# Kernel tuning notes

Measured on AMD Instinct MI355X. Metric: run time of the kernel, lower is better.

The kernel has to match this reference:

```python
import jax, jax.numpy as jnp
import numpy as np

B, T, DIM, H, HD = 1, 4096, 1024, 8, 128
ATTN_SCALE = 0.12


def _rms_norm(x):
    # F.rms_norm with default eps = finfo(dtype).eps, no learned weight
    eps = jnp.asarray(jnp.finfo(x.dtype).eps, x.dtype)
    return x * jax.lax.rsqrt(jnp.mean(x * x, axis=-1, keepdims=True) + eps)


def _rotary(x):
    # x: [B, T, H, D]; half-rotary: last D/2 freqs are zero (identity)
    t, d = x.shape[1], x.shape[-1]
    freqs = (1.0 / 1024.0) ** jnp.linspace(0.0, 1.0, d // 4, dtype=jnp.float32)
    freqs = jnp.concatenate([freqs, jnp.zeros(d // 4, dtype=jnp.float32)])
    theta = jnp.arange(t, dtype=jnp.float32)[:, None] * freqs[None, :]  # [T, D/2]
    cos = jnp.cos(theta)[None, :, None, :]
    sin = jnp.sin(theta)[None, :, None, :]
    x1, x2 = jnp.split(x.astype(jnp.float32), 2, axis=-1)
    y = jnp.concatenate([x1 * cos + x2 * sin, -x1 * sin + x2 * cos], axis=-1)
    return y.astype(x.dtype)


def setup_inputs() -> dict:
    key = jax.random.key(0)
    k1, k2, k3, k4, k5 = jax.random.split(key, 5)
    std = 0.5 * DIM ** -0.5
    bound = (3.0 ** 0.5) * std
    x = jax.random.normal(k1, (B, T, DIM), dtype=jnp.float32)
    ve = jax.random.normal(k2, (B, T, DIM), dtype=jnp.float32)
    qkv_w = jax.random.uniform(k3, (3, H * HD, DIM), dtype=jnp.float32,
                               minval=-bound, maxval=bound)
    lambdas = jnp.array([0.5, 0.5], dtype=jnp.float32)
    # c_proj is zero-initialized in the source; use small random weights so the
    # output (and gradients) are non-trivial for correctness testing
    c_proj_w = jax.random.normal(k4, (DIM, H * HD), dtype=jnp.float32) * 0.02
    docs = jnp.sort(jax.random.randint(k5, (T,), 0, 8, dtype=jnp.int32))
    return {"x": x, "ve": ve, "qkv_w": qkv_w, "lambdas": lambdas,
            "c_proj_w": c_proj_w, "docs": docs}


def reference(x, ve, qkv_w, lambdas, c_proj_w, docs):
    b, t, _ = x.shape
    w = qkv_w.reshape(3 * H * HD, -1)              # [3*hdim, dim]
    qkv = (x @ w.T).reshape(b, t, 3, H, HD)        # chunk(3, dim=-2) == axis 2 here
    q, k, v = qkv[:, :, 0], qkv[:, :, 1], qkv[:, :, 2]
    q, k = _rms_norm(q), _rms_norm(k)
    q, k = _rotary(q), _rotary(k)
    v = lambdas[0] * v + lambdas[1] * ve.reshape(v.shape)
    # doc-causal mask: attend within the same document, causally
    i = jnp.arange(t)
    mask = (i[:, None] >= i[None, :]) & (docs[:, None] == docs[None, :])  # [T, T]
    scores = jnp.einsum('bihd,bjhd->bhij', q, k) * ATTN_SCALE
    scores = jnp.where(mask[None, None], scores, -jnp.inf)
    p = jax.nn.softmax(scores, axis=-1)
    y = jnp.einsum('bhij,bjhd->bihd', p, v).reshape(b, t, H * HD)
    return y @ c_proj_w.T
```

## Files before the change

### kernel.cpp

```cpp
#include <hip/hip_runtime.h>
#include <hip/hip_bf16.h>
#include <cstdint>

typedef __attribute__((ext_vector_type(8))) short sh8;
typedef __attribute__((ext_vector_type(4))) float f4;
typedef __attribute__((ext_vector_type(16))) float f16v;

#define T_SEQ 4096
#define DIMN  1024
#define NH    8
#define HDIM  128
#define NQKV  3072
#define ATTN_SCALE 0.12f

__device__ __forceinline__ ushort f2bf(float x) {
  __hip_bfloat16 b = __float2bfloat16(x);
  return *reinterpret_cast<ushort*>(&b);
}
__device__ __forceinline__ float bf2f(ushort u) {
  uint v = ((uint)u) << 16;
  float f;
  __builtin_memcpy(&f, &v, 4);
  return f;
}

#define GLDS16(g, l) \
  __builtin_amdgcn_global_load_lds((const __attribute__((address_space(1))) void*)(g), \
                                   (__attribute__((address_space(3))) void*)(l), 16, 0, 0)

template <int N>
__device__ __forceinline__ void wait_vmcnt() {
  if constexpr (N == 0)      asm volatile("s_waitcnt vmcnt(0)" ::: "memory");
  else if constexpr (N == 4) asm volatile("s_waitcnt vmcnt(4)" ::: "memory");
  else if constexpr (N == 8) asm volatile("s_waitcnt vmcnt(8)" ::: "memory");
  __builtin_amdgcn_sched_barrier(0);
}
#define BAR __builtin_amdgcn_s_barrier()

__global__ __launch_bounds__(256) void k_prep(const float* __restrict__ x,
                                              const float* __restrict__ qw,
                                              const float* __restrict__ cw,
                                              ushort* __restrict__ xb, ushort* __restrict__ wb,
                                              ushort* __restrict__ cbuf,
                                              const int* __restrict__ docs, int* __restrict__ dstart) {
  const int b = blockIdx.x;
  if (b < 8192) {
    const int i = b * 256 + threadIdx.x;
    const float* src;
    ushort* dst;
    int j;
    if (i < 1048576)       { src = x;  dst = xb;   j = i; }
    else if (i < 1835008)  { src = qw; dst = wb;   j = i - 1048576; }
    else                   { src = cw; dst = cbuf; j = i - 1835008; }
    float4 v = reinterpret_cast<const float4*>(src)[j];
    ushort4 o;
    o.x = f2bf(v.x); o.y = f2bf(v.y); o.z = f2bf(v.z); o.w = f2bf(v.w);
    reinterpret_cast<ushort4*>(dst)[j] = o;
  } else {
    const int i = (b - 8192) * 256 + threadIdx.x;
    if (i < T_SEQ) {
      int d = docs[i];
      int lo = 0, hi = i;
      while (lo < hi) { int mid = (lo + hi) >> 1; if (docs[mid] < d) lo = mid + 1; else hi = mid; }
      dstart[i] = lo;
    }
  }
}

__global__ __launch_bounds__(512, 2) void k_gemm256(const ushort* __restrict__ A,
                                                    const ushort* __restrict__ B,
                                                    ushort* __restrict__ C,
                                                    int N, int K) {
  __shared__ ushort lds[2][512 * 64];
  const int tid = threadIdx.x;
  const int lane = tid & 63;
  const int w = tid >> 6;
  const int l5 = lane >> 5;
  const int lr32 = lane & 31;
  const int wave_m = w >> 2, wave_n = w & 3;

  const int nb = (blockIdx.x & 7) * 24 + (blockIdx.x >> 3);
  const int m0 = (nb / 12) * 256;
  const int n0 = (nb % 12) * 256;

  f16v acc[4][2];
#pragma unroll
  for (int i = 0; i < 4; ++i)
#pragma unroll
    for (int j = 0; j < 2; ++j)
#pragma unroll
      for (int r = 0; r < 16; ++r) acc[i][j][r] = 0.f;

  const int NT = K >> 6;

  auto STAGE4 = [&](int buf, int t, int ug) {
    const int k0 = t << 6;
#pragma unroll
    for (int uu = 0; uu < 4; ++uu) {
      const int u = ug * 4 + uu;
      const int row = u * 64 + (tid >> 3);
      const int c = (tid & 7) ^ (row & 7);
      const ushort* src = (row < 256 ? A + (size_t)(m0 + row) * K
                                     : B + (size_t)(n0 + row - 256) * K) + k0 + c * 8;
      GLDS16(src, (char*)&lds[buf][0] + u * 8192 + w * 1024);
    }
  };

  STAGE4(0, 0, 0); STAGE4(0, 0, 1);
  wait_vmcnt<0>();
  BAR;

  int cur = 0;
  for (int t = 0; t < NT; ++t) {
    const bool more = (t + 1) < NT;
    const char* bb = (const char*)&lds[cur][0];

#define RD6(ks, a, b)                                                              \
    _Pragma("unroll") for (int mt = 0; mt < 4; ++mt) {                             \
      const int row = wave_m * 128 + mt * 32 + lr32;                               \
      a[mt] = *(const sh8*)(bb + row * 128 + ((((ks) * 2 + l5) ^ (row & 7)) * 16));\
    }                                                                              \
    _Pragma("unroll") for (int nt = 0; nt < 2; ++nt) {                             \
      const int row = 256 + wave_n * 64 + nt * 32 + lr32;                          \
      b[nt] = *(const sh8*)(bb + row * 128 + ((((ks) * 2 + l5) ^ (row & 7)) * 16));\
    }

#define MFMA8(a, b)                                                                \
    __builtin_amdgcn_s_setprio(1);                                                 \
    _Pragma("unroll") for (int mt = 0; mt < 4; ++mt)                               \
    _Pragma("unroll") for (int nt = 0; nt < 2; ++nt)                               \
      acc[mt][nt] = __builtin_amdgcn_mfma_f32_32x32x16_bf16(a[mt], b[nt],          \
                                                            acc[mt][nt], 0, 0, 0); \
    __builtin_amdgcn_s_setprio(0);

    {
      sh8 a[4], b[2];
      RD6(0, a, b)
      if (more) STAGE4(cur ^ 1, t + 1, 0);
      MFMA8(a, b)
    }
    {
      sh8 a[4], b[2];
      RD6(1, a, b)
      if (more) STAGE4(cur ^ 1, t + 1, 1);
      MFMA8(a, b)
    }
    BAR;
    {
      sh8 a[4], b[2];
      RD6(2, a, b)
      MFMA8(a, b)
    }
    {
      sh8 a[4], b[2];
      RD6(3, a, b)
      MFMA8(a, b)
    }
    if (more) wait_vmcnt<0>();
    BAR;
    cur ^= 1;
  }
#undef RD6
#undef MFMA8

#pragma unroll
  for (int mt = 0; mt < 4; ++mt)
#pragma unroll
    for (int nt = 0; nt < 2; ++nt) {
      const int gcol = n0 + wave_n * 64 + nt * 32 + lr32;
#pragma unroll
      for (int r = 0; r < 16; ++r) {
        const int grow = m0 + wave_m * 128 + mt * 32 + (r & 3) + 8 * (r >> 2) + 4 * l5;
        C[(size_t)grow * N + gcol] = f2bf(acc[mt][nt][r]);
      }
    }
}

__global__ __launch_bounds__(256) void k_gemm2(const ushort* __restrict__ A,
                                               const ushort* __restrict__ B,
                                               float* __restrict__ C,
                                               int N, int K, int gx) {
  constexpr int BM = 128, BN = 128;
  constexpr int CHA = BM * 4;
  constexpr int TILEB = (BM + BN) * 64;

  __shared__ __attribute__((aligned(16))) char lds[3 * TILEB];

  const int tid = threadIdx.x;
  const int lane = tid & 63;
  const int w = tid >> 6;
  const int l5 = lane >> 5;
  const int lr32 = lane & 31;
  const int wm = w >> 1, wn = w & 1;

  const int nwg = gridDim.x;
  const int nb = (blockIdx.x & 7) * (nwg >> 3) + (blockIdx.x >> 3);
  const int m0 = (nb / gx) * BM;
  const int n0 = (nb % gx) * BN;

  f16v acc[2][2];
#pragma unroll
  for (int i = 0; i < 2; ++i)
#pragma unroll
    for (int j = 0; j < 2; ++j)
#pragma unroll
      for (int r = 0; r < 16; ++r) acc[i][j][r] = 0.f;

  const int NT = K >> 5;

  auto STAGE = [&](int t, int buf) {
    const int k0 = t << 5;
#pragma unroll
    for (int l = 0; l < 4; ++l) {
      const int cb = (l * 4 + w) * 64;
      const int ch = cb + lane;
      const ushort* src;
      if (ch < CHA) {
        const int row = ch >> 2;
        const int cs = (ch & 3) ^ ((row >> 1) & 3);
        src = A + (size_t)(m0 + row) * K + k0 + cs * 8;
      } else {
        const int c2 = ch - CHA;
        const int row = c2 >> 2;
        const int cs = (c2 & 3) ^ ((row >> 1) & 3);
        src = B + (size_t)(n0 + row) * K + k0 + cs * 8;
      }
      GLDS16(src, lds + buf * TILEB + cb * 16);
    }
  };

  STAGE(0, 0);
  STAGE(1, 1);
  wait_vmcnt<4>();
  BAR;

  int bufc = 0;
  for (int t = 0; t < NT; ++t) {
    const bool more = (t + 2) < NT;
    if (more) STAGE(t + 2, bufc == 0 ? 2 : (bufc == 1 ? 0 : 1));

    const char* bb = lds + bufc * TILEB;
#pragma unroll
    for (int ks = 0; ks < 2; ++ks) {
      sh8 a[2], b[2];
#pragma unroll
      for (int mt = 0; mt < 2; ++mt) {
        const int row = wm * 64 + mt * 32 + lr32;
        a[mt] = *(const sh8*)(bb + row * 64 + (((ks * 2 + l5) ^ ((row >> 1) & 3)) * 16));
      }
#pragma unroll
      for (int nt = 0; nt < 2; ++nt) {
        const int row = wn * 64 + nt * 32 + lr32;
        b[nt] = *(const sh8*)(bb + BM * 64 + row * 64 + (((ks * 2 + l5) ^ ((row >> 1) & 3)) * 16));
      }
      __builtin_amdgcn_s_setprio(1);
#pragma unroll
      for (int mt = 0; mt < 2; ++mt)
#pragma unroll
        for (int nt = 0; nt < 2; ++nt)
          acc[mt][nt] = __builtin_amdgcn_mfma_f32_32x32x16_bf16(a[mt], b[nt], acc[mt][nt], 0, 0, 0);
      __builtin_amdgcn_s_setprio(0);
    }

    if (more) wait_vmcnt<4>();
    else      wait_vmcnt<0>();
    BAR;
    bufc = bufc == 2 ? 0 : bufc + 1;
  }

#pragma unroll
  for (int mt = 0; mt < 2; ++mt)
#pragma unroll
    for (int nt = 0; nt < 2; ++nt) {
      const int gcol = n0 + wn * 64 + nt * 32 + lr32;
#pragma unroll
      for (int r = 0; r < 16; ++r) {
        const int grow = m0 + wm * 64 + mt * 32 + (r & 3) + 8 * (r >> 2) + 4 * l5;
        __builtin_nontemporal_store(acc[mt][nt][r], &C[(size_t)grow * N + gcol]);
      }
    }
}

__global__ __launch_bounds__(256) void k_fuse(const ushort* __restrict__ qkvb,
                                              const float* __restrict__ ve,
                                              const float* __restrict__ lam,
                                              ushort* __restrict__ qh, ushort* __restrict__ kh,
                                              ushort* __restrict__ vh) {
  const int pair = blockIdx.x * 4 + (threadIdx.x >> 6);
  const int t = pair >> 3, h = pair & 7;
  const int l = threadIdx.x & 63;
  const ushort* base = qkvb + (size_t)t * NQKV + h * HDIM + 2 * l;
  uint qu = *reinterpret_cast<const uint*>(base);
  uint ku = *reinterpret_cast<const uint*>(base + 1024);
  uint vu = *reinterpret_cast<const uint*>(base + 2048);
  float q0 = bf2f((ushort)qu), q1 = bf2f((ushort)(qu >> 16));
  float k0 = bf2f((ushort)ku), k1 = bf2f((ushort)(ku >> 16));
  float v0 = bf2f((ushort)vu), v1 = bf2f((ushort)(vu >> 16));
  float sq = q0 * q0 + q1 * q1, sk = k0 * k0 + k1 * k1;
#pragma unroll
  for (int m = 1; m < 64; m <<= 1) { sq += __shfl_xor(sq, m); sk += __shfl_xor(sk, m); }
  const float eps = 1.1920928955078125e-07f;
  float rq = rsqrtf(sq * (1.f / 128.f) + eps);
  float rk = rsqrtf(sk * (1.f / 128.f) + eps);
  q0 *= rq; q1 *= rq; k0 *= rk; k1 *= rk;
  float c0 = 1.f, s0 = 0.f, c1 = 1.f, s1 = 0.f;
  if ((l & 31) < 16) {
    const int f0 = 2 * (l & 31);
    float fr0 = exp2f(-10.f * (float)f0 * (1.f / 31.f));
    float fr1 = exp2f(-10.f * (float)(f0 + 1) * (1.f / 31.f));
    sincosf((float)t * fr0, &s0, &c0);
    sincosf((float)t * fr1, &s1, &c1);
  }
  float qx0 = __shfl_xor(q0, 32), qx1 = __shfl_xor(q1, 32);
  float kx0 = __shfl_xor(k0, 32), kx1 = __shfl_xor(k1, 32);
  const float sgn = (l < 32) ? 1.f : -1.f;
  float qr0 = q0 * c0 + sgn * qx0 * s0;
  float qr1 = q1 * c1 + sgn * qx1 * s1;
  float kr0 = k0 * c0 + sgn * kx0 * s0;
  float kr1 = k1 * c1 + sgn * kx1 * s1;
  const float l0 = lam[0], l1 = lam[1];
  float2 vev = *reinterpret_cast<const float2*>(ve + (size_t)t * DIMN + h * HDIM + 2 * l);
  float vr0 = l0 * v0 + l1 * vev.x;
  float vr1 = l0 * v1 + l1 * vev.y;
  const size_t o = ((size_t)h * T_SEQ + t) * HDIM + 2 * l;
  *reinterpret_cast<uint*>(qh + o) = (uint)f2bf(qr0) | ((uint)f2bf(qr1) << 16);
  *reinterpret_cast<uint*>(kh + o) = (uint)f2bf(kr0) | ((uint)f2bf(kr1) << 16);
  *reinterpret_cast<uint*>(vh + o) = (uint)f2bf(vr0) | ((uint)f2bf(vr1) << 16);
}

__global__ __launch_bounds__(256) void k_vt(const ushort* __restrict__ vh, ushort* __restrict__ vt) {
  const int tb = blockIdx.x, db = blockIdx.y, h = blockIdx.z;
  __shared__ ushort L[64][68];
  const int tid = threadIdx.x;
  const int t0 = tb * 64, d0 = db * 64;
  const size_t ib = ((size_t)h * T_SEQ + t0) * HDIM + d0;
#pragma unroll
  for (int p = 0; p < 4; ++p) {
    const int row = p * 16 + (tid >> 4);
    const int c4 = (tid & 15) * 4;
    ushort4 v = *reinterpret_cast<const ushort4*>(vh + ib + (size_t)row * HDIM + c4);
    *reinterpret_cast<ushort4*>(&L[row][c4]) = v;
  }
  __syncthreads();
  const size_t ob = ((size_t)h * HDIM + d0) * T_SEQ + t0;
#pragma unroll
  for (int p = 0; p < 4; ++p) {
    const int drow = p * 16 + (tid >> 4);
    const int t4 = (tid & 15) * 4;
    ushort4 v;
    v.x = L[t4 + 0][drow]; v.y = L[t4 + 1][drow];
    v.z = L[t4 + 2][drow]; v.w = L[t4 + 3][drow];
    *reinterpret_cast<ushort4*>(vt + ob + (size_t)drow * T_SEQ + t4) = v;
  }
}

__global__ __launch_bounds__(256) void k_attn(const ushort* __restrict__ qh,
                                              const ushort* __restrict__ kh,
                                              const ushort* __restrict__ vt,
                                              const int* __restrict__ doc_start,
                                              ushort* __restrict__ y) {
  const int h  = blockIdx.x;
  const int qb = blockIdx.y;
  const int q0 = qb * 64;
  const int tid  = threadIdx.x;
  const int wave = tid >> 6;
  const int lane = tid & 63;
  const int lr = lane & 15, lg = lane >> 4;

  __shared__ ushort Ks[2][64 * 128];
  __shared__ ushort Vs[2][128 * 64];
  __shared__ ushort Ps[4][16 * 64];

  const ushort* Kg = kh + (size_t)h * T_SEQ * HDIM;
  const ushort* Vg = vt + (size_t)h * HDIM * T_SEQ;

  const int i_me = q0 + wave * 16 + lr;
  sh8 qf[4];
  {
    const ushort* qp = qh + ((size_t)h * T_SEQ + i_me) * HDIM + lg * 8;
#pragma unroll
    for (int c = 0; c < 4; ++c) qf[c] = *reinterpret_cast<const sh8*>(qp + c * 32);
  }
  const int ds_me = doc_start[i_me];
  const int ds_hi = doc_start[q0 + 63];
  const int kb0   = doc_start[q0] >> 6;

  const f4 fzero = {0.f, 0.f, 0.f, 0.f};
  f4 o_acc[8];
#pragma unroll
  for (int i = 0; i < 8; ++i) o_acc[i] = fzero;
  float m_me = -1e30f, l_me = 0.f;

  auto STAGE = [&](int b, int k0) {
#pragma unroll
    for (int p = 0; p < 4; ++p) {
      const int c = p * 256 + tid;
      const int row = c >> 4, cc = c & 15;
      GLDS16(Kg + (size_t)(k0 + row) * HDIM + (cc ^ (row & 7)) * 8,
             &Ks[b][(p * 256 + wave * 64) * 8]);
    }
#pragma unroll
    for (int p = 0; p < 4; ++p) {
      const int c = p * 256 + tid;
      const int d = c >> 3, cc = c & 7;
      GLDS16(Vg + (size_t)d * T_SEQ + k0 + (cc ^ (d & 7)) * 8,
             &Vs[b][(p * 256 + wave * 64) * 8]);
    }
  };

  int cur = 0;
  STAGE(0, kb0 * 64);

  const int sw = (lr & 7) << 4;

  for (int kb = kb0; kb <= qb; ++kb) {
    const int k0 = kb * 64;
    __syncthreads();
    if (kb < qb) STAGE(cur ^ 1, k0 + 64);

    const char* Kb = (const char*)&Ks[cur][0];
    const char* Vb = (const char*)&Vs[cur][0];
    char* Pw = (char*)&Ps[wave][0];

    f4 sacc[4];
#pragma unroll
    for (int jt = 0; jt < 4; ++jt) sacc[jt] = fzero;
#pragma unroll
    for (int jt = 0; jt < 4; ++jt)
#pragma unroll
      for (int c = 0; c < 4; ++c) {
        sh8 kf = *reinterpret_cast<const sh8*>(Kb + (jt * 16 + lr) * 256 + ((c * 64 + lg * 16) ^ sw));
        sacc[jt] = __builtin_amdgcn_mfma_f32_16x16x32_bf16(kf, qf[c], sacc[jt], 0, 0, 0);
      }

    const bool fullblk = (kb < qb) && (ds_hi <= k0);
    float p[4][4];
#pragma unroll
    for (int jt = 0; jt < 4; ++jt)
#pragma unroll
      for (int r = 0; r < 4; ++r) {
        float s = sacc[jt][r] * ATTN_SCALE;
        const int j = k0 + jt * 16 + lg * 4 + r;
        bool valid = fullblk || ((j <= i_me) && (j >= ds_me));
        p[jt][r] = valid ? s : -1e30f;
      }
    float tm = -1e30f;
#pragma unroll
    for (int jt = 0; jt < 4; ++jt) {
      float a = fmaxf(p[jt][0], p[jt][1]), b = fmaxf(p[jt][2], p[jt][3]);
      tm = fmaxf(tm, fmaxf(a, b));
    }
    tm = fmaxf(tm, __shfl_xor(tm, 16));
    tm = fmaxf(tm, __shfl_xor(tm, 32));
    const float mnew = fmaxf(m_me, tm);
    const float sc = __expf(m_me - mnew);
    m_me = mnew;
    float rs = 0.f;
#pragma unroll
    for (int jt = 0; jt < 4; ++jt)
#pragma unroll
      for (int r = 0; r < 4; ++r) {
        float pv = __expf(p[jt][r] - mnew);
        p[jt][r] = pv;
        rs += pv;
      }
    rs += __shfl_xor(rs, 16);
    rs += __shfl_xor(rs, 32);
    l_me = l_me * sc + rs;

#pragma unroll
    for (int jt = 0; jt < 4; ++jt) {
      uint2 u;
      u.x = (uint)f2bf(p[jt][0]) | ((uint)f2bf(p[jt][1]) << 16);
      u.y = (uint)f2bf(p[jt][2]) | ((uint)f2bf(p[jt][3]) << 16);
      *reinterpret_cast<uint2*>(Pw + lr * 128 + ((jt * 32 + lg * 8) ^ sw)) = u;
    }

    float sco[4];
#pragma unroll
    for (int rr = 0; rr < 4; ++rr) sco[rr] = __shfl(sc, lg * 4 + rr);
#pragma unroll
    for (int dt = 0; dt < 8; ++dt)
#pragma unroll
      for (int rr = 0; rr < 4; ++rr) o_acc[dt][rr] *= sco[rr];

#pragma unroll
    for (int ks = 0; ks < 2; ++ks) {
      sh8 pa = *reinterpret_cast<const sh8*>(Pw + lr * 128 + ((ks * 64 + lg * 16) ^ sw));
#pragma unroll
      for (int dt = 0; dt < 8; ++dt) {
        sh8 vf = *reinterpret_cast<const sh8*>(Vb + (dt * 16 + lr) * 128 + ((ks * 64 + lg * 16) ^ sw));
        o_acc[dt] = __builtin_amdgcn_mfma_f32_16x16x32_bf16(pa, vf, o_acc[dt], 0, 0, 0);
      }
    }

    __builtin_amdgcn_s_barrier();
    cur ^= 1;
  }

  float lo[4];
#pragma unroll
  for (int rr = 0; rr < 4; ++rr) lo[rr] = __shfl(l_me, lg * 4 + rr);
#pragma unroll
  for (int dt = 0; dt < 8; ++dt)
#pragma unroll
    for (int rr = 0; rr < 4; ++rr) {
      const int trow = q0 + wave * 16 + lg * 4 + rr;
      y[(size_t)trow * DIMN + h * HDIM + dt * 16 + lr] = f2bf(o_acc[dt][rr] / lo[rr]);
    }
}

extern "C" void kernel_launch(void* const* d_in, const int* in_sizes, int n_in,
                              void* d_out, int out_size, void* d_ws, size_t ws_size,
                              hipStream_t stream) {
  const float* x    = (const float*)d_in[0];
  const float* ve   = (const float*)d_in[1];
  const float* qkvw = (const float*)d_in[2];
  const float* lam  = (const float*)d_in[3];
  const float* cpw  = (const float*)d_in[4];
  const int*   docs = (const int*)d_in[5];
  float* out = (float*)d_out;
  char* ws = (char*)d_ws;

  ushort* qkvb = (ushort*)(ws);
  ushort* xb   = (ushort*)(ws + (24ull << 20));
  ushort* wb   = (ushort*)(ws + (32ull << 20));
  ushort* cb   = (ushort*)(ws + (38ull << 20));
  ushort* qh   = (ushort*)(ws + (40ull << 20));
  ushort* kh   = (ushort*)(ws + (48ull << 20));
  ushort* vh   = (ushort*)(ws + (56ull << 20));
  ushort* vt   = (ushort*)(ws + (64ull << 20));
  ushort* yb   = (ushort*)(ws + (72ull << 20));
  int*  dstart = (int*)(ws + (80ull << 20));

  k_prep<<<8192 + 16, 256, 0, stream>>>(x, qkvw, cpw, xb, wb, cb, docs, dstart);

  k_gemm256<<<192, 512, 0, stream>>>(xb, wb, qkvb, NQKV, DIMN);

  k_fuse<<<T_SEQ * NH / 4, 256, 0, stream>>>(qkvb, ve, lam, qh, kh, vh);
  k_vt<<<dim3(T_SEQ / 64, HDIM / 64, NH), 256, 0, stream>>>(vh, vt);

  k_attn<<<dim3(NH, T_SEQ / 64), 256, 0, stream>>>(qh, kh, vt, dstart, yb);

  k_gemm2<<<256, 256, 0, stream>>>(yb, cb, out, DIMN, DIMN, DIMN / 128);
}
```

Baseline: 107.9 us.

## Rewrite QKV GEMM with 256x192 tiles, 16x16 MFMA and 8-phase pipelined loads

Replaces the 256x256-tile QKV projection GEMM with a 256x192-tile variant launched on 256 blocks, so the grid covers all 256 CUs instead of 192. It switches from 32x32x16 to 16x16x32 MFMA with a new LDS read pattern and precomputed global pointers. Loads for the next K-tile are split into groups interleaved across four compute phases, with finer vmcnt waits and barriers. The extra barriers and lgkmcnt waits add synchronization overhead, and the smaller N tile lowers data reuse per block.

```diff
diff --git a/kernel.cpp b/kernel.cpp
--- a/kernel.cpp
+++ b/kernel.cpp
@@ -31,10 +31,13 @@
 template <int N>
 __device__ __forceinline__ void wait_vmcnt() {
   if constexpr (N == 0)      asm volatile("s_waitcnt vmcnt(0)" ::: "memory");
+  else if constexpr (N == 2) asm volatile("s_waitcnt vmcnt(2)" ::: "memory");
+  else if constexpr (N == 3) asm volatile("s_waitcnt vmcnt(3)" ::: "memory");
   else if constexpr (N == 4) asm volatile("s_waitcnt vmcnt(4)" ::: "memory");
   else if constexpr (N == 8) asm volatile("s_waitcnt vmcnt(8)" ::: "memory");
   __builtin_amdgcn_sched_barrier(0);
 }
+#define LGKM0 do { asm volatile("s_waitcnt lgkmcnt(0)" ::: "memory"); __builtin_amdgcn_sched_barrier(0); } while (0)
 #define BAR __builtin_amdgcn_s_barrier()
 
 __global__ __launch_bounds__(256) void k_prep(const float* __restrict__ x,
@@ -67,111 +70,103 @@
   }
 }
 
-__global__ __launch_bounds__(512, 2) void k_gemm256(const ushort* __restrict__ A,
-                                                    const ushort* __restrict__ B,
-                                                    ushort* __restrict__ C,
-                                                    int N, int K) {
-  __shared__ ushort lds[2][512 * 64];
+__global__ __launch_bounds__(512, 2) void k_gemm8p(const ushort* __restrict__ A,
+                                                   const ushort* __restrict__ B,
+                                                   ushort* __restrict__ C,
+                                                   int N, int K) {
+  __shared__ ushort lds[2][448 * 64];
   const int tid = threadIdx.x;
   const int lane = tid & 63;
   const int w = tid >> 6;
-  const int l5 = lane >> 5;
-  const int lr32 = lane & 31;
+  const int lr = lane & 15, lg = lane >> 4;
   const int wave_m = w >> 2, wave_n = w & 3;
 
-  const int nb = (blockIdx.x & 7) * 24 + (blockIdx.x >> 3);
-  const int m0 = (nb / 12) * 256;
-  const int n0 = (nb % 12) * 256;
-
-  f16v acc[4][2];
-#pragma unroll
-  for (int i = 0; i < 4; ++i)
-#pragma unroll
-    for (int j = 0; j < 2; ++j)
-#pragma unroll
-      for (int r = 0; r < 16; ++r) acc[i][j][r] = 0.f;
+  const int nb = (blockIdx.x & 7) * 32 + (blockIdx.x >> 3);
+  const int m0 = (nb >> 4) * 256;
+  const int n0 = (nb & 15) * 192;
+
+  const ushort* pb[7];
+#pragma unroll
+  for (int G = 0; G < 7; ++G) {
+    const int idx = G * 512 + w * 64 + lane;
+    const int row = idx >> 3;
+    const int c = (lane & 7) ^ (row & 7);
+    pb[G] = (row < 256 ? A + (size_t)(m0 + row) * K
+                       : B + (size_t)(n0 + row - 256) * K) + c * 8;
+  }
+
+  f4 acc[8][3];
+  const f4 fzero = {0.f, 0.f, 0.f, 0.f};
+#pragma unroll
+  for (int i = 0; i < 8; ++i)
+#pragma unroll
+    for (int j = 0; j < 3; ++j) acc[i][j] = fzero;
 
   const int NT = K >> 6;
 
-  auto STAGE4 = [&](int buf, int t, int ug) {
-    const int k0 = t << 6;
-#pragma unroll
-    for (int uu = 0; uu < 4; ++uu) {
-      const int u = ug * 4 + uu;
-      const int row = u * 64 + (tid >> 3);
-      const int c = (tid & 7) ^ (row & 7);
-      const ushort* src = (row < 256 ? A + (size_t)(m0 + row) * K
-                                     : B + (size_t)(n0 + row - 256) * K) + k0 + c * 8;
-      GLDS16(src, (char*)&lds[buf][0] + u * 8192 + w * 1024);
-    }
+  auto SG = [&](int buf, int t, int G) {
+    GLDS16(pb[G] + (t << 6), (char*)&lds[buf][0] + (G * 512 + w * 64) * 16);
   };
 
-  STAGE4(0, 0, 0); STAGE4(0, 0, 1);
-  wait_vmcnt<0>();
+#define RDA(dst, mh, kkh, bp)                                                       \
+  _Pragma("unroll") for (int mf = 0; mf < 4; ++mf) {                                \
+    const int row_ = wave_m * 128 + (mh) * 64 + mf * 16 + lr;                       \
+    dst[mf] = *(const sh8*)((bp) + row_ * 128 + ((((kkh) * 4 + lg) ^ (lr & 7)) * 16)); \
+  }
+#define RDB(dst, kkh, bp)                                                           \
+  _Pragma("unroll") for (int nf = 0; nf < 3; ++nf) {                                \
+    const int row_ = 256 + wave_n * 48 + nf * 16 + lr;                              \
+    dst[nf] = *(const sh8*)((bp) + row_ * 128 + ((((kkh) * 4 + lg) ^ (lr & 7)) * 16)); \
+  }
+#define MM12(mh, a, b)                                                              \
+  __builtin_amdgcn_s_setprio(1);                                                    \
+  _Pragma("unroll") for (int mf = 0; mf < 4; ++mf)                                  \
+  _Pragma("unroll") for (int nf = 0; nf < 3; ++nf)                                  \
+    acc[(mh) * 4 + mf][nf] = __builtin_amdgcn_mfma_f32_16x16x32_bf16(               \
+        a[mf], b[nf], acc[(mh) * 4 + mf][nf], 0, 0, 0);                             \
+  __builtin_amdgcn_s_setprio(0);
+
+  SG(0, 0, 0); SG(0, 0, 1); SG(0, 0, 4); SG(0, 0, 5); SG(0, 0, 6); SG(0, 0, 2); SG(0, 0, 3);
+  wait_vmcnt<2>();
   BAR;
 
-  int cur = 0;
   for (int t = 0; t < NT; ++t) {
+    const int buf = t & 1;
+    const char* bp = (const char*)&lds[buf][0];
     const bool more = (t + 1) < NT;
-    const char* bb = (const char*)&lds[cur][0];
-
-#define RD6(ks, a, b)                                                              \
-    _Pragma("unroll") for (int mt = 0; mt < 4; ++mt) {                             \
-      const int row = wave_m * 128 + mt * 32 + lr32;                               \
-      a[mt] = *(const sh8*)(bb + row * 128 + ((((ks) * 2 + l5) ^ (row & 7)) * 16));\
-    }                                                                              \
-    _Pragma("unroll") for (int nt = 0; nt < 2; ++nt) {                             \
-      const int row = 256 + wave_n * 64 + nt * 32 + lr32;                          \
-      b[nt] = *(const sh8*)(bb + row * 128 + ((((ks) * 2 + l5) ^ (row & 7)) * 16));\
-    }
-
-#define MFMA8(a, b)                                                                \
-    __builtin_amdgcn_s_setprio(1);                                                 \
-    _Pragma("unroll") for (int mt = 0; mt < 4; ++mt)                               \
-    _Pragma("unroll") for (int nt = 0; nt < 2; ++nt)                               \
-      acc[mt][nt] = __builtin_amdgcn_mfma_f32_32x32x16_bf16(a[mt], b[nt],          \
-                                                            acc[mt][nt], 0, 0, 0); \
-    __builtin_amdgcn_s_setprio(0);
-
-    {
-      sh8 a[4], b[2];
-      RD6(0, a, b)
-      if (more) STAGE4(cur ^ 1, t + 1, 0);
-      MFMA8(a, b)
-    }
-    {
-      sh8 a[4], b[2];
-      RD6(1, a, b)
-      if (more) STAGE4(cur ^ 1, t + 1, 1);
-      MFMA8(a, b)
-    }
-    BAR;
-    {
-      sh8 a[4], b[2];
-      RD6(2, a, b)
-      MFMA8(a, b)
-    }
-    {
-      sh8 a[4], b[2];
-      RD6(3, a, b)
-      MFMA8(a, b)
-    }
-    if (more) wait_vmcnt<0>();
-    BAR;
-    cur ^= 1;
-  }
-#undef RD6
-#undef MFMA8
-
-#pragma unroll
-  for (int mt = 0; mt < 4; ++mt)
-#pragma unroll
-    for (int nt = 0; nt < 2; ++nt) {
-      const int gcol = n0 + wave_n * 64 + nt * 32 + lr32;
-#pragma unroll
-      for (int r = 0; r < 16; ++r) {
-        const int grow = m0 + wave_m * 128 + mt * 32 + (r & 3) + 8 * (r >> 2) + 4 * l5;
-        C[(size_t)grow * N + gcol] = f2bf(acc[mt][nt][r]);
+    sh8 a0[4], a1[4], b0[3], b1[3];
+
+    RDA(a0, 0, 0, bp) RDB(b0, 0, bp)
+    if (more) { SG(buf ^ 1, t + 1, 0); SG(buf ^ 1, t + 1, 1); SG(buf ^ 1, t + 1, 4);
+                wait_vmcnt<3>(); }
+    else      { wait_vmcnt<0>(); }
+    BAR; LGKM0; MM12(0, a0, b0) BAR;
+
+    RDA(a1, 1, 0, bp)
+    if (more) { SG(buf ^ 1, t + 1, 5); SG(buf ^ 1, t + 1, 6); SG(buf ^ 1, t + 1, 2); }
+    BAR; LGKM0; MM12(1, a1, b0) BAR;
+
+    RDA(a0, 0, 1, bp) RDB(b1, 1, bp)
+    if (more) SG(buf ^ 1, t + 1, 3);
+    BAR; LGKM0; MM12(0, a0, b1) BAR;
+
+    RDA(a1, 1, 1, bp)
+    if (more) wait_vmcnt<2>();
+    BAR; LGKM0; MM12(1, a1, b1) BAR;
+  }
+#undef RDA
+#undef RDB
+#undef MM12
+
+#pragma unroll
+  for (int mf = 0; mf < 8; ++mf)
+#pragma unroll
+    for (int nf = 0; nf < 3; ++nf) {
+      const int gcol = n0 + wave_n * 48 + nf * 16 + lr;
+#pragma unroll
+      for (int r = 0; r < 4; ++r) {
+        const int grow = m0 + wave_m * 128 + mf * 16 + lg * 4 + r;
+        C[(size_t)grow * N + gcol] = f2bf(acc[mf][nf][r]);
       }
     }
 }
@@ -535,7 +530,7 @@
 
   k_prep<<<8192 + 16, 256, 0, stream>>>(x, qkvw, cpw, xb, wb, cb, docs, dstart);
 
-  k_gemm256<<<192, 512, 0, stream>>>(xb, wb, qkvb, NQKV, DIMN);
+  k_gemm8p<<<256, 512, 0, stream>>>(xb, wb, qkvb, NQKV, DIMN);
 
   k_fuse<<<T_SEQ * NH / 4, 256, 0, stream>>>(qkvb, ve, lam, qh, kh, vh);
   k_vt<<<dim3(T_SEQ / 64, HDIM / 64, NH), 256, 0, stream>>>(vh, vt);
```

Result: faster. 104.1 us (-3.5%).
